# Optimization experiments

Hardware: AMD Instinct MI355X
Metric: run time of the kernel (lower is better)

## Reference

```python
import jax, jax.numpy as jnp
import numpy as np
import math

FACTOR = 5  # self.factor


def setup_inputs() -> dict:
    key = jax.random.key(0)
    kq, kk, kv = jax.random.split(key, 3)
    B, L, H, D = 4, 2048, 8, 64
    return {
        "queries": jax.random.normal(kq, (B, L, H, D), dtype=jnp.float32),
        "keys": jax.random.normal(kk, (B, L, H, D), dtype=jnp.float32),
        "values": jax.random.normal(kv, (B, L, H, D), dtype=jnp.float32),
        "attn_mask": jnp.zeros((1,), dtype=jnp.int32),  # unused by the module's forward
    }


def _prob_attention(queries, keys, values):
    B, L_Q, H, D = queries.shape
    L_K = keys.shape[1]
    # to (B, H, L, D)
    Q = queries.transpose(0, 2, 1, 3)
    K = keys.transpose(0, 2, 1, 3)
    V = values.transpose(0, 2, 1, 3)

    U_part = min(FACTOR * int(math.ceil(math.log(L_K))), L_K)  # sample_k
    u = min(FACTOR * int(math.ceil(math.log(L_Q))), L_Q)       # n_top

    # --- _prob_QE: sampled QK, sparsity measure M, top-u query selection ---
    idx_key = jax.random.key(42)  # fixed key stands in for torch.randint
    index_sample = jax.random.randint(idx_key, (L_Q, U_part), 0, L_K)  # [L_Q, S]
    K_sample = K[:, :, index_sample, :]                                # [B,H,L_Q,S,E]
    Q_K_sample = jnp.einsum('bhqe,bhqse->bhqs', Q, K_sample)           # [B,H,L_Q,S]
    M = Q_K_sample.max(axis=-1) - Q_K_sample.sum(axis=-1) / L_K        # [B,H,L_Q]
    M_top = jax.lax.top_k(M, u)[1]                                     # [B,H,u]

    Q_reduce = jnp.take_along_axis(Q, M_top[..., None], axis=2)        # [B,H,u,E]
    scores = jnp.einsum('bhue,bhke->bhuk', Q_reduce, K)                # [B,H,u,L_K]
    scores = scores * (1.0 / math.sqrt(D))                             # scale=None -> 1/sqrt(D)

    # --- initial context (mask_flag=True path): mean of V over keys ---
    context = jnp.broadcast_to(V.mean(axis=2, keepdims=True), (B, H, L_Q, D))

    attn = jax.nn.softmax(scores, axis=-1)
    context_update = jnp.einsum('bhuk,bhkd->bhud', attn, V)            # [B,H,u,D]

    # scatter the updated rows back at the selected query positions
    b = jnp.arange(B)[:, None, None]
    h = jnp.arange(H)[None, :, None]
    context = context.at[b, h, M_top].set(context_update)

    return context.transpose(0, 2, 1, 3)  # [B, L_Q, H, D]


def reference(queries, keys, values, attn_mask):
    # attn_mask is accepted but unused by the torch module's mask_flag=True path
    return _prob_attention(queries, keys, values)
```

## Files before the change

### kernel.cpp

```cpp
#include <hip/hip_runtime.h>
#include <stdint.h>


static constexpr int Bc = 4, Lc = 2048, Hc = 8, Dc = 64, NUc = 40;
static constexpr int NCH = 32, CHK = 64;
static constexpr int UT = 10;

struct TF2 { uint32_t a, b; };

__host__ __device__ constexpr uint32_t rotl32c(uint32_t x, int r) {
    return (x << r) | (x >> (32 - r));
}

__host__ __device__ constexpr TF2 tf2x32c(uint32_t k0, uint32_t k1, uint32_t x0, uint32_t x1) {
    uint32_t ks[3] = {k0, k1, k0 ^ k1 ^ 0x1BD11BDAu};
    const int R0[4] = {13, 15, 26, 6};
    const int R1[4] = {17, 29, 16, 24};
    x0 += ks[0];
    x1 += ks[1];
    for (int i = 0; i < 5; ++i) {
        const int* R = (i & 1) ? R1 : R0;
        for (int j = 0; j < 4; ++j) {
            x0 += x1;
            x1 = rotl32c(x1, R[j]);
            x1 ^= x0;
        }
        x0 += ks[(i + 1) % 3];
        x1 += ks[(i + 2) % 3] + (uint32_t)(i + 1);
    }
    return TF2{x0, x1};
}

__global__ __launch_bounds__(256) void k_index(int* __restrict__ idx) {
    constexpr TF2 K2 = tf2x32c(0u, 42u, 0u, 1u);
    int j = blockIdx.x * 256 + threadIdx.x;
    TF2 r = tf2x32c(K2.a, K2.b, 0u, (uint32_t)j);
    idx[j] = (int)((r.a ^ r.b) & 2047u);
}

__global__ __launch_bounds__(256, 4) void k_M(const float* __restrict__ Q,
                                              const float* __restrict__ K,
                                              const int* __restrict__ idxg,
                                              float* __restrict__ M) {
    int lane = threadIdx.x & 63;
    int w = threadIdx.x >> 6;
    int blk = blockIdx.x;
    int xcd = blk & 7;
    int local = blk >> 3;
    int b = xcd >> 1;
    int q = (xcd & 1) * 1024 + local * 4 + w;
    int h = lane >> 3;
    int myidx = (lane < 40) ? idxg[q * 40 + lane] : 0;

    const float4* Q4 = reinterpret_cast<const float4*>(Q);
    const float4* K4 = reinterpret_cast<const float4*>(K);
    size_t qb = (size_t)(b * Lc + q) * 128;
    float4 qv0 = Q4[qb + 2 * lane];
    float4 qv1 = Q4[qb + 2 * lane + 1];

    float mx8[8], sm8[8];
#pragma unroll
    for (int j = 0; j < 8; ++j) { mx8[j] = -INFINITY; sm8[j] = 0.f; }
#pragma unroll
    for (int i = 0; i < 5; ++i) {
#pragma unroll
        for (int j = 0; j < 8; ++j) {
            int kk = __shfl(myidx, i * 8 + j, 64);
            size_t rb = (size_t)(b * Lc + kk) * 128;
            float4 kv0 = K4[rb + 2 * lane];
            float4 kv1 = K4[rb + 2 * lane + 1];
            float pv = qv0.x * kv0.x + qv0.y * kv0.y + qv0.z * kv0.z + qv0.w * kv0.w +
                       qv1.x * kv1.x + qv1.y * kv1.y + qv1.z * kv1.z + qv1.w * kv1.w;
#pragma unroll
            for (int m = 1; m < 8; m <<= 1) pv += __shfl_xor(pv, m, 64);
            mx8[j] = fmaxf(mx8[j], pv);
            sm8[j] += pv;
        }
    }
    float mx = mx8[0], sm = sm8[0];
#pragma unroll
    for (int j = 1; j < 8; ++j) { mx = fmaxf(mx, mx8[j]); sm += sm8[j]; }
    if ((lane & 7) == 0) M[(b * 8 + h) * Lc + q] = mx - sm * (1.0f / 2048.0f);
}

__global__ __launch_bounds__(256) void k_topk(const float* __restrict__ M, int* __restrict__ top,
                                              uint32_t* __restrict__ gmask) {
    __shared__ uint32_t hist[256];
    __shared__ uint32_t sh_bin, sh_need;
    __shared__ int sel[NUc];
    __shared__ int tie[128];
    __shared__ uint32_t selCnt, tieCnt;
    int bh = blockIdx.x;
    int t = threadIdx.x;
    uint32_t uk[8];
#pragma unroll
    for (int i = 0; i < 8; ++i) {
        uint32_t s = __float_as_uint(M[bh * Lc + i * 256 + t]);
        uk[i] = (s & 0x80000000u) ? ~s : (s | 0x80000000u);
    }
    uint32_t prefix = 0, need = NUc;
    for (int pass = 0; pass < 4; ++pass) {
        int shift = 24 - 8 * pass;
        hist[t] = 0;
        __syncthreads();
#pragma unroll
        for (int i = 0; i < 8; ++i) {
            bool ok = (pass == 0) || ((uk[i] >> (shift + 8)) == prefix);
            if (ok) atomicAdd(&hist[(uk[i] >> shift) & 255u], 1u);
        }
        __syncthreads();
        if (t < 64) {
            uint32_t c0 = hist[4 * t], c1 = hist[4 * t + 1];
            uint32_t c2 = hist[4 * t + 2], c3 = hist[4 * t + 3];
            uint32_t s = c0 + c1 + c2 + c3;
            uint32_t suf = s;
#pragma unroll
            for (int m = 1; m < 64; m <<= 1) {
                uint32_t o = __shfl_down(suf, m, 64);
                if (t + m < 64) suf += o;
            }
            uint32_t above = suf - s;
            if (suf >= need && above < need) {
                uint32_t rem = need - above;
                uint32_t bsel, cnt;
                if (c3 >= rem) { bsel = 4 * t + 3; cnt = rem; }
                else if (c3 + c2 >= rem) { bsel = 4 * t + 2; cnt = rem - c3; }
                else if (c3 + c2 + c1 >= rem) { bsel = 4 * t + 1; cnt = rem - c3 - c2; }
                else { bsel = 4 * t; cnt = rem - c3 - c2 - c1; }
                sh_bin = bsel;
                sh_need = cnt;
            }
        }
        __syncthreads();
        prefix = (pass == 0) ? sh_bin : ((prefix << 8) | sh_bin);
        need = sh_need;
        __syncthreads();
    }
    const uint32_t T = prefix;
    if (t == 0) { selCnt = 0; tieCnt = 0; }
    __syncthreads();
#pragma unroll
    for (int i = 0; i < 8; ++i) {
        int idx = i * 256 + t;
        if (uk[i] > T) {
            uint32_t slot = atomicAdd(&selCnt, 1u);
            if (slot < NUc) sel[slot] = idx;
        } else if (uk[i] == T) {
            uint32_t slot = atomicAdd(&tieCnt, 1u);
            if (slot < 128) tie[slot] = idx;
        }
    }
    __syncthreads();
    if (t == 0) {
        int n = (int)tieCnt;
        if (n > 128) n = 128;
        for (int a = 1; a < n; ++a) {
            int key = tie[a], c = a - 1;
            while (c >= 0 && tie[c] > key) { tie[c + 1] = tie[c]; --c; }
            tie[c + 1] = key;
        }
        uint32_t base = selCnt;
        for (uint32_t j = 0; j < need && base + j < NUc; ++j) sel[base + j] = tie[j];
    }
    __syncthreads();
    if (t < NUc) top[bh * NUc + t] = sel[t];
    if (t < 64) {
        uint32_t word = 0;
#pragma unroll
        for (int j = 0; j < NUc; ++j) {
            int s = sel[j];
            if ((s >> 5) == t) word |= 1u << (s & 31);
        }
        gmask[bh * 64 + t] = word;
    }
}

__global__ __launch_bounds__(64, 4) void k_attn_part(const float* __restrict__ Q,
                                                     const float* __restrict__ K,
                                                     const float* __restrict__ V,
                                                     const int* __restrict__ top,
                                                     float* __restrict__ wsO,
                                                     float* __restrict__ wsm,
                                                     float* __restrict__ wsl,
                                                     float* __restrict__ vpart) {
    __shared__ float Qs[UT][64];
    __shared__ float pT[64][12];
    __shared__ int tqs[UT];
    int blk = blockIdx.x;
    int xcd = blk & 7, local = blk >> 3;
    int bh = xcd * 4 + (local >> 7);
    int rem = local & 127;
    int chunk = rem >> 2, ut = rem & 3;
    int b = bh >> 3, h = bh & 7;
    int t = threadIdx.x;

    if (t < UT) tqs[t] = top[bh * NUc + ut * UT + t];
    __syncthreads();
#pragma unroll
    for (int j = 0; j < UT; ++j)
        Qs[j][t] = Q[(((size_t)(b * Lc + tqs[j])) * Hc + h) * Dc + t];
    __syncthreads();

    int kg = chunk * CHK + t;
    const float4* Kr = reinterpret_cast<const float4*>(&K[(((size_t)(b * Lc + kg)) * Hc + h) * Dc]);
    float acc[UT];
#pragma unroll
    for (int u = 0; u < UT; ++u) acc[u] = 0.f;
#pragma unroll
    for (int i = 0; i < 16; ++i) {
        float4 kv = Kr[i];
#pragma unroll
        for (int u = 0; u < UT; ++u) {
            float4 qv = *reinterpret_cast<const float4*>(&Qs[u][i * 4]);
            acc[u] += qv.x * kv.x + qv.y * kv.y + qv.z * kv.z + qv.w * kv.w;
        }
    }
#pragma unroll
    for (int u = 0; u < UT; ++u) acc[u] *= 0.125f;
    float mr[UT];
#pragma unroll
    for (int u = 0; u < UT; ++u) {
        float v = acc[u];
#pragma unroll
        for (int m = 1; m < 64; m <<= 1) v = fmaxf(v, __shfl_xor(v, m, 64));
        mr[u] = v;
    }
    float pr[UT];
#pragma unroll
    for (int u = 0; u < UT; ++u) {
        pr[u] = __expf(acc[u] - mr[u]);
        pT[t][u] = pr[u];
    }
    float sr[UT];
#pragma unroll
    for (int u = 0; u < UT; ++u) {
        float v = pr[u];
#pragma unroll
        for (int m = 1; m < 64; m <<= 1) v += __shfl_xor(v, m, 64);
        sr[u] = v;
    }
    int sbase = (bh * NCH + chunk) * NUc + ut * UT;
#pragma unroll
    for (int u = 0; u < UT; ++u) {
        if (t == u) {
            wsm[sbase + u] = mr[u];
            wsl[sbase + u] = sr[u];
        }
    }
    __syncthreads();
#pragma unroll
    for (int u = 0; u < UT; ++u) acc[u] = 0.f;
    float vs = 0.f;
    const float* Vbh = V + ((size_t)b * Lc * Hc + h) * Dc;
    for (int k = 0; k < 64; ++k) {
        float vv = Vbh[(size_t)(chunk * CHK + k) * 512 + t];
        vs += vv;
        float4 pa = *reinterpret_cast<const float4*>(&pT[k][0]);
        float4 pb = *reinterpret_cast<const float4*>(&pT[k][4]);
        float2 pc = *reinterpret_cast<const float2*>(&pT[k][8]);
        acc[0] += pa.x * vv; acc[1] += pa.y * vv; acc[2] += pa.z * vv; acc[3] += pa.w * vv;
        acc[4] += pb.x * vv; acc[5] += pb.y * vv; acc[6] += pb.z * vv; acc[7] += pb.w * vv;
        acc[8] += pc.x * vv; acc[9] += pc.y * vv;
    }
    if (ut == 0) vpart[(bh * NCH + chunk) * 64 + t] = vs;
    size_t obase = (size_t)(bh * NCH + chunk) * 2560 + (size_t)(ut * UT) * 64;
#pragma unroll
    for (int u = 0; u < UT; ++u) wsO[obase + u * 64 + t] = acc[u];
}

__global__ __launch_bounds__(256) void k_attn_comb(const float* __restrict__ wsO,
                                                   const float* __restrict__ wsm,
                                                   const float* __restrict__ wsl,
                                                   const float* __restrict__ vpart,
                                                   float* __restrict__ stage,
                                                   float* __restrict__ vm) {
    __shared__ float cm[NCH][5], cl[NCH][5], cf[NCH][5];
    int blk = blockIdx.x;
    int ut = blk & 7, bh = blk >> 3;
    int t = threadIdx.x;
    for (int i = t; i < NCH * 5; i += 256) {
        int c = i / 5, j = i % 5;
        cm[c][j] = wsm[(bh * NCH + c) * NUc + ut * 5 + j];
        cl[c][j] = wsl[(bh * NCH + c) * NUc + ut * 5 + j];
    }
    __syncthreads();
    if (t < 5) {
        float m = -INFINITY;
#pragma unroll
        for (int c = 0; c < NCH; ++c) m = fmaxf(m, cm[c][t]);
        float L = 0.f;
#pragma unroll
        for (int c = 0; c < NCH; ++c) {
            float f = __expf(cm[c][t] - m);
            L += cl[c][t] * f;
            cf[c][t] = f;
        }
        float inv = 1.0f / L;
#pragma unroll
        for (int c = 0; c < NCH; ++c) cf[c][t] *= inv;
    }
    if (ut == 0 && t >= 64 && t < 128) {
        int d = t - 64;
        float s = 0.f;
#pragma unroll
        for (int c = 0; c < NCH; ++c) s += vpart[(bh * NCH + c) * 64 + d];
        vm[bh * 64 + d] = s * (1.0f / 2048.0f);
    }
    __syncthreads();
    for (int i = t; i < 5 * 64; i += 256) {
        int j = i >> 6, d = i & 63;
        float val = 0.f;
#pragma unroll
        for (int c = 0; c < NCH; ++c)
            val += wsO[((size_t)(bh * NCH + c)) * 2560 + (ut * 5 + j) * 64 + d] * cf[c][j];
        stage[(size_t)bh * 2560 + (ut * 5 + j) * 64 + d] = val;
    }
}

__global__ void k_out(const float* __restrict__ stage, const float* __restrict__ vm,
                      const int* __restrict__ top, const uint32_t* __restrict__ gmask,
                      float* __restrict__ out) {
    int o4 = blockIdx.x * blockDim.x + threadIdx.x;
    if (o4 >= Bc * Lc * Hc * (Dc / 4)) return;
    int dq = o4 & 15;
    int h = (o4 >> 4) & 7;
    int bl = o4 >> 7;
    int b = bl >> 11, l = bl & 2047;
    int bh = b * 8 + h;
    float4 v;
    uint32_t wmask = gmask[bh * 64 + (l >> 5)];
    if ((wmask >> (l & 31)) & 1u) {
        int u = 0;
#pragma unroll
        for (int j = 0; j < NUc; ++j)
            if (top[bh * NUc + j] == l) u = j;
        v = reinterpret_cast<const float4*>(stage)[(bh * NUc + u) * 16 + dq];
    } else {
        v = reinterpret_cast<const float4*>(vm)[bh * 16 + dq];
    }
    reinterpret_cast<float4*>(out)[o4] = v;
}

extern "C" void kernel_launch(void* const* d_in, const int* in_sizes, int n_in,
                              void* d_out, int out_size, void* d_ws, size_t ws_size,
                              hipStream_t stream) {
    (void)in_sizes; (void)n_in; (void)out_size; (void)ws_size;
    const float* Q = (const float*)d_in[0];
    const float* K = (const float*)d_in[1];
    const float* V = (const float*)d_in[2];
    float* out = (float*)d_out;

    float* wsO   = (float*)d_out;
    float* wsm   = (float*)((char*)d_out + 10485760);
    float* wsl   = (float*)((char*)d_out + 10649600);
    float* vpart = (float*)((char*)d_out + 10813440);
    float* M     = (float*)((char*)d_out + 11075584);
    int*   idxg  = (int*)((char*)d_out + 11337728);
    int*      top   = (int*)d_ws;
    float*    stage = (float*)((char*)d_ws + 8192);
    float*    vm    = (float*)((char*)d_ws + 335872);
    uint32_t* gmask = (uint32_t*)((char*)d_ws + 344064);

    hipLaunchKernelGGL(k_index, dim3(320), dim3(256), 0, stream, idxg);
    hipLaunchKernelGGL(k_M, dim3(2048), dim3(256), 0, stream, Q, K, idxg, M);
    hipLaunchKernelGGL(k_topk, dim3(Bc * Hc), dim3(256), 0, stream, M, top, gmask);
    hipLaunchKernelGGL(k_attn_part, dim3(4096), dim3(64), 0, stream, Q, K, V, top,
                       wsO, wsm, wsl, vpart);
    hipLaunchKernelGGL(k_attn_comb, dim3(Bc * Hc * 8), dim3(256), 0, stream, wsO, wsm, wsl,
                       vpart, stage, vm);
    hipLaunchKernelGGL(k_out, dim3(4096), dim3(256), 0, stream, stage, vm, top, gmask, out);
}
```

Before: 96.32 us.

## Fuse index generation into k_M, atomically reduce V mean, merge combine into output

Computes the random sample indices inline in k_M, which removes the k_index launch. The V-mean partial sums are accumulated with atomicAdd into vm, which k_M zeroes first; this replaces the vpart buffer and its reduction. When the workspace is large enough, the split-softmax combine is folded into the output kernel: each selected row recomputes its rescale factors and reduces over the chunks, so the separate k_comb launch is dropped. The intent is fewer launches and less intermediate traffic. The cost is redundant combine work per selected row, float atomic ordering nondeterminism, and the path choice now depends on the workspace size.

```diff
diff --git a/kernel.cpp b/kernel.cpp
--- a/kernel.cpp
+++ b/kernel.cpp
@@ -31,26 +31,25 @@
     return TF2{x0, x1};
 }
 
-__global__ __launch_bounds__(256) void k_index(int* __restrict__ idx) {
-    constexpr TF2 K2 = tf2x32c(0u, 42u, 0u, 1u);
-    int j = blockIdx.x * 256 + threadIdx.x;
-    TF2 r = tf2x32c(K2.a, K2.b, 0u, (uint32_t)j);
-    idx[j] = (int)((r.a ^ r.b) & 2047u);
-}
-
 __global__ __launch_bounds__(256, 4) void k_M(const float* __restrict__ Q,
                                               const float* __restrict__ K,
-                                              const int* __restrict__ idxg,
-                                              float* __restrict__ M) {
+                                              float* __restrict__ M,
+                                              float* __restrict__ vm) {
+    constexpr TF2 K2 = tf2x32c(0u, 42u, 0u, 1u);
     int lane = threadIdx.x & 63;
     int w = threadIdx.x >> 6;
     int blk = blockIdx.x;
+    if (blk < 8) vm[blk * 256 + threadIdx.x] = 0.f;
     int xcd = blk & 7;
     int local = blk >> 3;
     int b = xcd >> 1;
     int q = (xcd & 1) * 1024 + local * 4 + w;
     int h = lane >> 3;
-    int myidx = (lane < 40) ? idxg[q * 40 + lane] : 0;
+    int myidx = 0;
+    if (lane < 40) {
+        TF2 r = tf2x32c(K2.a, K2.b, 0u, (uint32_t)(q * 40 + lane));
+        myidx = (int)((r.a ^ r.b) & 2047u);
+    }
 
     const float4* Q4 = reinterpret_cast<const float4*>(Q);
     const float4* K4 = reinterpret_cast<const float4*>(K);
@@ -182,7 +181,7 @@
                                                      float* __restrict__ wsO,
                                                      float* __restrict__ wsm,
                                                      float* __restrict__ wsl,
-                                                     float* __restrict__ vpart) {
+                                                     float* __restrict__ vm) {
     __shared__ float Qs[UT][64];
     __shared__ float pT[64][12];
     __shared__ int tqs[UT];
@@ -262,18 +261,63 @@
         acc[4] += pb.x * vv; acc[5] += pb.y * vv; acc[6] += pb.z * vv; acc[7] += pb.w * vv;
         acc[8] += pc.x * vv; acc[9] += pc.y * vv;
     }
-    if (ut == 0) vpart[(bh * NCH + chunk) * 64 + t] = vs;
+    if (ut == 0) atomicAdd(&vm[bh * 64 + t], vs * (1.0f / 2048.0f));
     size_t obase = (size_t)(bh * NCH + chunk) * 2560 + (size_t)(ut * UT) * 64;
 #pragma unroll
     for (int u = 0; u < UT; ++u) wsO[obase + u * 64 + t] = acc[u];
 }
 
-__global__ __launch_bounds__(256) void k_attn_comb(const float* __restrict__ wsO,
-                                                   const float* __restrict__ wsm,
-                                                   const float* __restrict__ wsl,
-                                                   const float* __restrict__ vpart,
-                                                   float* __restrict__ stage,
-                                                   float* __restrict__ vm) {
+__global__ void k_out_inl(const float* __restrict__ wsO, const float* __restrict__ wsm,
+                          const float* __restrict__ wsl, const float* __restrict__ vm,
+                          const int* __restrict__ top, const uint32_t* __restrict__ gmask,
+                          float* __restrict__ out) {
+    int o4 = blockIdx.x * blockDim.x + threadIdx.x;
+    if (o4 >= Bc * Lc * Hc * (Dc / 4)) return;
+    int dq = o4 & 15;
+    int h = (o4 >> 4) & 7;
+    int bl = o4 >> 7;
+    int b = bl >> 11, l = bl & 2047;
+    int bh = b * 8 + h;
+    float4 v;
+    uint32_t wmask = gmask[bh * 64 + (l >> 5)];
+    if ((wmask >> (l & 31)) & 1u) {
+        int u = 0;
+#pragma unroll
+        for (int j = 0; j < NUc; ++j)
+            if (top[bh * NUc + j] == l) u = j;
+        float cf[NCH];
+        float m = -INFINITY;
+#pragma unroll
+        for (int c = 0; c < NCH; ++c) {
+            cf[c] = wsm[(bh * NCH + c) * NUc + u];
+            m = fmaxf(m, cf[c]);
+        }
+        float L = 0.f;
+#pragma unroll
+        for (int c = 0; c < NCH; ++c) {
+            float e = __expf(cf[c] - m);
+            L += wsl[(bh * NCH + c) * NUc + u] * e;
+            cf[c] = e;
+        }
+        const float4* W4 = reinterpret_cast<const float4*>(wsO);
+        float4 a = make_float4(0.f, 0.f, 0.f, 0.f);
+#pragma unroll
+        for (int c = 0; c < NCH; ++c) {
+            float4 o = W4[(size_t)(bh * NCH + c) * 640 + u * 16 + dq];
+            a.x += o.x * cf[c]; a.y += o.y * cf[c]; a.z += o.z * cf[c]; a.w += o.w * cf[c];
+        }
+        float inv = 1.0f / L;
+        v = make_float4(a.x * inv, a.y * inv, a.z * inv, a.w * inv);
+    } else {
+        v = reinterpret_cast<const float4*>(vm)[bh * 16 + dq];
+    }
+    reinterpret_cast<float4*>(out)[o4] = v;
+}
+
+__global__ __launch_bounds__(256) void k_comb(const float* __restrict__ wsO,
+                                              const float* __restrict__ wsm,
+                                              const float* __restrict__ wsl,
+                                              float* __restrict__ stage) {
     __shared__ float cm[NCH][5], cl[NCH][5], cf[NCH][5];
     int blk = blockIdx.x;
     int ut = blk & 7, bh = blk >> 3;
@@ -298,13 +342,6 @@
         float inv = 1.0f / L;
 #pragma unroll
         for (int c = 0; c < NCH; ++c) cf[c][t] *= inv;
-    }
-    if (ut == 0 && t >= 64 && t < 128) {
-        int d = t - 64;
-        float s = 0.f;
-#pragma unroll
-        for (int c = 0; c < NCH; ++c) s += vpart[(bh * NCH + c) * 64 + d];
-        vm[bh * 64 + d] = s * (1.0f / 2048.0f);
     }
     __syncthreads();
     for (int i = t; i < 5 * 64; i += 256) {
@@ -344,29 +381,41 @@
 extern "C" void kernel_launch(void* const* d_in, const int* in_sizes, int n_in,
                               void* d_out, int out_size, void* d_ws, size_t ws_size,
                               hipStream_t stream) {
-    (void)in_sizes; (void)n_in; (void)out_size; (void)ws_size;
+    (void)in_sizes; (void)n_in; (void)out_size;
     const float* Q = (const float*)d_in[0];
     const float* K = (const float*)d_in[1];
     const float* V = (const float*)d_in[2];
     float* out = (float*)d_out;
 
-    float* wsO   = (float*)d_out;
-    float* wsm   = (float*)((char*)d_out + 10485760);
-    float* wsl   = (float*)((char*)d_out + 10649600);
-    float* vpart = (float*)((char*)d_out + 10813440);
-    float* M     = (float*)((char*)d_out + 11075584);
-    int*   idxg  = (int*)((char*)d_out + 11337728);
     int*      top   = (int*)d_ws;
-    float*    stage = (float*)((char*)d_ws + 8192);
-    float*    vm    = (float*)((char*)d_ws + 335872);
-    uint32_t* gmask = (uint32_t*)((char*)d_ws + 344064);
-
-    hipLaunchKernelGGL(k_index, dim3(320), dim3(256), 0, stream, idxg);
-    hipLaunchKernelGGL(k_M, dim3(2048), dim3(256), 0, stream, Q, K, idxg, M);
-    hipLaunchKernelGGL(k_topk, dim3(Bc * Hc), dim3(256), 0, stream, M, top, gmask);
-    hipLaunchKernelGGL(k_attn_part, dim3(4096), dim3(64), 0, stream, Q, K, V, top,
-                       wsO, wsm, wsl, vpart);
-    hipLaunchKernelGGL(k_attn_comb, dim3(Bc * Hc * 8), dim3(256), 0, stream, wsO, wsm, wsl,
-                       vpart, stage, vm);
-    hipLaunchKernelGGL(k_out, dim3(4096), dim3(256), 0, stream, stage, vm, top, gmask, out);
-}
+    float*    vm    = (float*)((char*)d_ws + 8192);
+    uint32_t* gmask = (uint32_t*)((char*)d_ws + 16384);
+    float* M = (float*)((char*)d_out + 11075584);
+
+    const bool bigws = ws_size >= 11534336;
+
+    if (bigws) {
+        float* wsm = (float*)((char*)d_ws + 32768);
+        float* wsl = (float*)((char*)d_ws + 196608);
+        float* wsO = (float*)((char*)d_ws + 393216);
+        hipLaunchKernelGGL(k_M, dim3(2048), dim3(256), 0, stream, Q, K, M, vm);
+        hipLaunchKernelGGL(k_topk, dim3(Bc * Hc), dim3(256), 0, stream, M, top, gmask);
+        hipLaunchKernelGGL(k_attn_part, dim3(4096), dim3(64), 0, stream, Q, K, V, top,
+                           wsO, wsm, wsl, vm);
+        hipLaunchKernelGGL(k_out_inl, dim3(4096), dim3(256), 0, stream, wsO, wsm, wsl, vm,
+                           top, gmask, out);
+    } else {
+        float* wsO   = (float*)d_out;
+        float* wsm   = (float*)((char*)d_out + 10485760);
+        float* wsl   = (float*)((char*)d_out + 10649600);
+        float* stage = (float*)((char*)d_ws + 24576);
+        hipLaunchKernelGGL(k_M, dim3(2048), dim3(256), 0, stream, Q, K, M, vm);
+        hipLaunchKernelGGL(k_topk, dim3(Bc * Hc), dim3(256), 0, stream, M, top, gmask);
+        hipLaunchKernelGGL(k_attn_part, dim3(4096), dim3(64), 0, stream, Q, K, V, top,
+                           wsO, wsm, wsl, vm);
+        hipLaunchKernelGGL(k_comb, dim3(Bc * Hc * 8), dim3(256), 0, stream, wsO, wsm, wsl,
+                           stage);
+        hipLaunchKernelGGL(k_out, dim3(4096), dim3(256), 0, stream, stage, vm, top, gmask,
+                           out);
+    }
+}
```

Result: faster. 91.96 us (-4.5%).
